# Kernel optimization log

Measured on AMD Instinct MI355X. Metric: run time of the kernel, lower is better.

The kernel has to match this reference:

```python
import jax, jax.numpy as jnp
import numpy as np

B, N, C, H, NC, P = 16, 577, 768, 12, 8, 576  # batch, seq(=patches+cls), dim, heads, curves, patches
D = C // H


def setup_inputs() -> dict:
    key = jax.random.key(0)
    ks = jax.random.split(key, 8)
    x = jax.random.normal(ks[0], (B, N, C), jnp.float32)
    qkv_w = jax.random.normal(ks[1], (C, 3 * C), jnp.float32) * 0.02
    proj_w = jax.random.normal(ks[2], (C, C), jnp.float32) * 0.02
    proj_b = jnp.zeros((C,), jnp.float32)
    # learned per-head decay logits; +3 so sigmoid ~0.95 (slow decay, realistic)
    ai_list = jax.random.normal(ks[3], (NC, H), jnp.float32) + 3.0
    mask_weights = jax.random.normal(ks[4], (NC,), jnp.float32) * 0.1 + 1.0 / NC
    normalize = 1.0 + 0.1 * jax.random.normal(ks[5], (H,), jnp.float32)
    # space-filling-curve inverse index permutations (one per curve)
    curve_inds = jnp.stack([
        jax.random.permutation(jax.random.fold_in(ks[6], c), P) for c in range(NC)
    ]).astype(jnp.int32)
    return dict(x=x, qkv_w=qkv_w, proj_w=proj_w, proj_b=proj_b,
                ai_list=ai_list, mask_weights=mask_weights,
                normalize=normalize, curve_inds=curve_inds)


def _build_mask(ai_list, mask_weights, curve_inds):
    # sigmoid(a)^|i-j| gathered by the curve permutation == sigmoid(a)^|ind_i - ind_j|
    a = jax.nn.sigmoid(ai_list)                                  # [NC,H]
    ci = curve_inds.astype(jnp.float32)                          # [NC,P]
    diff = jnp.abs(ci[:, :, None] - ci[:, None, :])              # [NC,P,P]
    Mc = a[:, :, None, None] ** diff[:, None, :, :]              # [NC,H,P,P]
    Mp = jnp.einsum('c,chpq->hpq', mask_weights, Mc)             # weighted sum over curves
    # cls-token row/col: each curve contributes ones -> sum of weights
    sw = jnp.sum(mask_weights)
    M = jnp.pad(Mp, ((0, 0), (1, 0), (1, 0)))                    # [H,N,N]
    M = M.at[:, 0, :].set(sw)
    M = M.at[:, :, 0].set(sw)
    return M


def reference(x, qkv_w, proj_w, proj_b, ai_list, mask_weights, normalize, curve_inds):
    qkv = (x @ qkv_w).reshape(B, N, 3, H, D)
    q = jnp.transpose(qkv[:, :, 0], (0, 2, 1, 3))                # [B,H,N,D]
    k = jnp.transpose(qkv[:, :, 1], (0, 2, 1, 3))
    v = jnp.transpose(qkv[:, :, 2], (0, 2, 1, 3))
    # NOTE: original overwrites self.scale with the bool `scale`=True -> multiply by 1
    attn = jnp.einsum('bhnd,bhmd->bhnm', q, k)                   # [B,H,N,N]
    M = _build_mask(ai_list, mask_weights, curve_inds)           # [H,N,N]
    attn = attn * M[None] * normalize[None, :, None, None]       # method='mul_v1'
    attn = jax.nn.softmax(attn, axis=-1)
    out = jnp.einsum('bhnm,bhmd->bhnd', attn, v)
    out = jnp.transpose(out, (0, 2, 1, 3)).reshape(B, N, C)
    return out @ proj_w + proj_b
```

## Files before the change

### kernel.cpp

```cpp
#include <hip/hip_runtime.h>


typedef _Float16 f16;
typedef _Float16 half8 __attribute__((ext_vector_type(8)));
typedef _Float16 half4 __attribute__((ext_vector_type(4)));
typedef float floatx4 __attribute__((ext_vector_type(4)));

#define DEVINL __device__ __forceinline__

#define Bb 16
#define NN 577
#define CC 768
#define HH 12
#define DD 64
#define MM (Bb * NN)
#define VTLD 584
#define MLD 580
#define CLD 136

DEVINL void async_copy16(void* lds, const void* g) {
  __builtin_amdgcn_global_load_lds(
      (const __attribute__((address_space(1))) void*)g,
      (__attribute__((address_space(3))) void*)lds, 16, 0, 0);
}

DEVINL half8 ld_swz(const f16* lds, int row, int chunk) {
  return *(const half8*)(lds + row * 64 + ((chunk ^ (row & 7)) << 3));
}

DEVINL int xcd_swizzle(int orig, int nwg) {
  int q = nwg >> 3, r = nwg & 7;
  int xcd = orig & 7, loc = orig >> 3;
  return (xcd < r ? xcd * (q + 1) : r * (q + 1) + (xcd - r) * q) + loc;
}

__global__ void cvt_kernel(const float* __restrict__ in, f16* __restrict__ out, int n) {
  int i = (blockIdx.x * blockDim.x + threadIdx.x) * 4;
  if (i >= n) return;
  float4 v = *(const float4*)(in + i);
  half4 o = {(f16)v.x, (f16)v.y, (f16)v.z, (f16)v.w};
  *(half4*)(out + i) = o;
}

__global__ void transpose_cvt(const float* __restrict__ in, f16* __restrict__ out,
                              int N3, int K) {
  __shared__ float t[32][33];
  const int k0 = blockIdx.x * 32, n0 = blockIdx.y * 32;
  const int tx = threadIdx.x & 31, ty = threadIdx.x >> 5;
#pragma unroll
  for (int p = 0; p < 4; ++p)
    t[ty + p * 8][tx] = in[(size_t)(k0 + ty + p * 8) * N3 + n0 + tx];
  __syncthreads();
#pragma unroll
  for (int p = 0; p < 4; ++p)
    out[(size_t)(n0 + ty + p * 8) * K + k0 + tx] = (f16)t[tx][ty + p * 8];
}

__global__ void mask_kernel(const float* __restrict__ ai, const float* __restrict__ mw,
                            const float* __restrict__ nrm, const int* __restrict__ ci,
                            float* __restrict__ Mb) {
  const int i = blockIdx.x;
  const int h = blockIdx.y;
  __shared__ float la_s[8], wv_s[8], cif[8], swn_s;
  int tid = threadIdx.x;
  if (tid < 8) {
    float av = ai[tid * 12 + h];
    float a = 1.f / (1.f + __expf(-av));
    la_s[tid] = __logf(a);
    wv_s[tid] = mw[tid];
    cif[tid] = (i > 0) ? (float)ci[tid * 576 + (i - 1)] : 0.f;
  }
  if (tid == 0) {
    float s = 0.f;
    for (int c = 0; c < 8; ++c) s += mw[c];
    swn_s = s * nrm[h] * 1.44269504088896f;
  }
  __syncthreads();
  const float nr = nrm[h] * 1.44269504088896f;
  float* row = Mb + ((size_t)h * NN + i) * MLD;
  for (int j = tid; j < NN; j += blockDim.x) {
    float val;
    if (i == 0 || j == 0) {
      val = swn_s;
    } else {
      float acc = 0.f;
#pragma unroll
      for (int c = 0; c < 8; ++c) {
        float d = fabsf(cif[c] - (float)ci[c * 576 + (j - 1)]);
        acc += wv_s[c] * __expf(la_s[c] * d);
      }
      val = acc * nr;
    }
    row[j] = val;
  }
}

DEVINL void gemm_mainloop(const f16* __restrict__ A, const f16* __restrict__ Bt,
                          int arow0, int brow0, int maxar,
                          f16* SMEM, floatx4 acc[4][4], int tid) {
  const int lane = tid & 63;
  const int wid = tid >> 6;
  const int wr = wid >> 1, wc = wid & 1;
  const int l15 = lane & 15, g = lane >> 4;
  const int r_ = tid >> 3, cp_ = tid & 7;
  const int lc_ = (cp_ ^ (r_ & 7)) << 3;

  auto stage = [&](f16* As, f16* Bs, int k0) {
#pragma unroll
    for (int q = 0; q < 4; ++q) {
      int idx = q * 256 + tid;
      int r = q * 32 + r_;
      int ar = arow0 + r; if (ar > maxar) ar = maxar;
      async_copy16(As + idx * 8, A + (size_t)ar * CC + k0 + lc_);
      async_copy16(Bs + idx * 8, Bt + (size_t)(brow0 + r) * CC + k0 + lc_);
    }
  };
  auto compute = [&](const f16* As, const f16* Bs) {
#pragma unroll
    for (int kk = 0; kk < 2; ++kk) {
      half8 af[4], bf[4];
#pragma unroll
      for (int mi = 0; mi < 4; ++mi) af[mi] = ld_swz(As, wr * 64 + mi * 16 + l15, kk * 4 + g);
#pragma unroll
      for (int ni = 0; ni < 4; ++ni) bf[ni] = ld_swz(Bs, wc * 64 + ni * 16 + l15, kk * 4 + g);
#pragma unroll
      for (int mi = 0; mi < 4; ++mi)
#pragma unroll
        for (int ni = 0; ni < 4; ++ni)
          acc[mi][ni] = __builtin_amdgcn_mfma_f32_16x16x32_f16(af[mi], bf[ni], acc[mi][ni], 0, 0, 0);
    }
  };

  const int nt = CC / 64;
  stage(SMEM, SMEM + 8192, 0);
#pragma unroll 1
  for (int t = 0; t < nt; ++t) {
    f16* cAs = (t & 1) ? SMEM + 16384 : SMEM;
    f16* cBs = (t & 1) ? SMEM + 24576 : SMEM + 8192;
    f16* nAs = (t & 1) ? SMEM : SMEM + 16384;
    f16* nBs = (t & 1) ? SMEM + 8192 : SMEM + 24576;
    if (t + 1 < nt) {
      stage(nAs, nBs, (t + 1) * 64);
      asm volatile("s_waitcnt vmcnt(8)" ::: "memory");
    } else {
      asm volatile("s_waitcnt vmcnt(0)" ::: "memory");
    }
    __builtin_amdgcn_s_barrier();
    __builtin_amdgcn_sched_barrier(0);
    compute(cAs, cBs);
    __builtin_amdgcn_s_barrier();
  }
}

__global__ __launch_bounds__(256, 2)
void gemm_qkv(const f16* __restrict__ A, const f16* __restrict__ Bt,
              f16* __restrict__ qb, f16* __restrict__ kb, f16* __restrict__ vt) {
  __shared__ __align__(16) f16 SMEM[32768];
  floatx4 acc[4][4] = {};
  const int nwg = 18 * 73;
  const int wgid = xcd_swizzle(blockIdx.y * gridDim.x + blockIdx.x, nwg);
  const int m0 = (wgid / 18) * 128, n0 = (wgid % 18) * 128;
  gemm_mainloop(A, Bt, m0, n0, MM - 1, SMEM, acc, threadIdx.x);
  const int tid = threadIdx.x, lane = tid & 63, wid = tid >> 6;
  const int wr = wid >> 1, wc = wid & 1, l15 = lane & 15, g = lane >> 4;
  const int t = n0 / CC;
  const int h0 = (n0 - t * CC) >> 6;
  if (t < 2) {
#pragma unroll
    for (int mi = 0; mi < 4; ++mi)
#pragma unroll
      for (int ni = 0; ni < 4; ++ni)
#pragma unroll
        for (int r = 0; r < 4; ++r)
          SMEM[(wr * 64 + mi * 16 + 4 * g + r) * CLD + wc * 64 + ni * 16 + l15] =
              (f16)acc[mi][ni][r];
    __syncthreads();
    f16* dst = (t == 0) ? qb : kb;
#pragma unroll
    for (int p = 0; p < 8; ++p) {
      int c = p * 256 + tid;
      int ml = c >> 4, n3c = (c & 15) << 3;
      int mg = m0 + ml;
      if (mg < MM) {
        int b = mg / NN, n = mg - b * NN;
        int h = h0 + (n3c >> 6), d0 = n3c & 63;
        half8 v = *(const half8*)(SMEM + ml * CLD + n3c);
        *(half8*)(dst + ((size_t)(b * HH + h) * NN + n) * DD + d0) = v;
      }
    }
  } else {
#pragma unroll
    for (int mi = 0; mi < 4; ++mi)
#pragma unroll
      for (int ni = 0; ni < 4; ++ni)
#pragma unroll
        for (int r = 0; r < 4; ++r)
          SMEM[(wc * 64 + ni * 16 + l15) * CLD + wr * 64 + mi * 16 + 4 * g + r] =
              (f16)acc[mi][ni][r];
    __syncthreads();
#pragma unroll
    for (int p = 0; p < 8; ++p) {
      int c = p * 256 + tid;
      int n3 = c >> 4, mc = (c & 15) << 3;
      int mg = m0 + mc;
      int h = h0 + (n3 >> 6), d = n3 & 63;
      half8 v = *(const half8*)(SMEM + n3 * CLD + mc);
      int b0 = mg / NN, b7 = (mg + 7) / NN;
      if (mg + 7 < MM && b0 == b7) {
        *(half8*)(vt + ((size_t)(b0 * HH + h) * DD + d) * VTLD + (mg - b0 * NN)) = v;
      } else {
#pragma unroll
        for (int e = 0; e < 8; ++e) {
          int m2 = mg + e;
          if (m2 < MM) {
            int b = m2 / NN;
            vt[((size_t)(b * HH + h) * DD + d) * VTLD + (m2 - b * NN)] = v[e];
          }
        }
      }
    }
  }
}

__global__ __launch_bounds__(256, 2)
void gemm_proj(const f16* __restrict__ A, const f16* __restrict__ Bt,
               const float* __restrict__ bias, float* __restrict__ out) {
  __shared__ __align__(16) f16 SMEM[32768];
  floatx4 acc[4][4] = {};
  const int nwg = 6 * 73;
  const int wgid = xcd_swizzle(blockIdx.y * gridDim.x + blockIdx.x, nwg);
  const int m0 = (wgid / 6) * 128, n0 = (wgid % 6) * 128;
  gemm_mainloop(A, Bt, m0, n0, MM - 1, SMEM, acc, threadIdx.x);
  const int lane = threadIdx.x & 63, wid = threadIdx.x >> 6;
  const int wr = wid >> 1, wc = wid & 1, l15 = lane & 15, g = lane >> 4;
#pragma unroll
  for (int mi = 0; mi < 4; ++mi)
#pragma unroll
    for (int ni = 0; ni < 4; ++ni)
#pragma unroll
      for (int r = 0; r < 4; ++r) {
        int m = m0 + wr * 64 + mi * 16 + 4 * g + r;
        if (m >= MM) continue;
        int n = n0 + wc * 64 + ni * 16 + l15;
        out[(size_t)m * CC + n] = acc[mi][ni][r] + bias[n];
      }
}

__global__ __launch_bounds__(256, 2)
void attn_kernel(const f16* __restrict__ qb, const f16* __restrict__ kb,
                 const f16* __restrict__ vt, const float* __restrict__ Mb,
                 f16* __restrict__ aout) {
  __shared__ f16 Ks[2][64 * 64];
  __shared__ f16 Vs[2][64 * 64];
  const int D0 = (blockIdx.z * gridDim.y + blockIdx.y) * gridDim.x + blockIdx.x;
  const int wgid = xcd_swizzle(D0, 5 * HH * Bb);
  const int it = wgid % 5;
  const int rem = wgid / 5;
  const int b = rem % Bb, h = rem / Bb;
  const int tid = threadIdx.x, lane = tid & 63, wid = tid >> 6;
  const int l15 = lane & 15, g = lane >> 4;
  const size_t bh = (size_t)b * HH + h;
  const f16* qbh = qb + bh * NN * DD;
  const f16* kbh = kb + bh * NN * DD;
  const f16* vbh = vt + bh * DD * VTLD;
  const float* Mh = Mb + (size_t)h * NN * MLD;
  const int row0w = it * 128 + wid * 32;

  half8 qB[2][2];
#pragma unroll
  for (int qt = 0; qt < 2; ++qt) {
    int qr = row0w + qt * 16 + l15; if (qr > NN - 1) qr = NN - 1;
    const f16* qp = qbh + (size_t)qr * DD + g * 8;
    qB[qt][0] = *(const half8*)qp;
    qB[qt][1] = *(const half8*)(qp + 32);
  }
  const float* Mrow0;
  const float* Mrow1;
  {
    int r0 = row0w + l15;      if (r0 > NN - 1) r0 = NN - 1;
    int r1 = row0w + 16 + l15; if (r1 > NN - 1) r1 = NN - 1;
    Mrow0 = Mh + (size_t)r0 * MLD + 4 * g;
    Mrow1 = Mh + (size_t)r1 * MLD + 4 * g;
  }

  floatx4 acc[2][4] = {};
  float lsum[2] = {0.f, 0.f};
  float mrun[2] = {-3e38f, -3e38f};

  auto stage = [&](f16* Kd, f16* Vd, int j0) {
#pragma unroll
    for (int qi = 0; qi < 2; ++qi) {
      int idx = qi * 256 + tid;
      int r = idx >> 3, cp = idx & 7;
      int lc = (cp ^ (r & 7)) << 3;
      int j = j0 + r; if (j > NN - 1) j = NN - 1;
      async_copy16(Kd + idx * 8, kbh + (size_t)j * DD + lc);
      async_copy16(Vd + idx * 8, vbh + (size_t)r * VTLD + j0 + lc);
    }
  };
  auto ldmask = [&](floatx4 m4[2][4], int j0) {
#pragma unroll
    for (int jt = 0; jt < 4; ++jt) {
      m4[0][jt] = *(const floatx4*)(Mrow0 + j0 + jt * 16);
      m4[1][jt] = *(const floatx4*)(Mrow1 + j0 + jt * 16);
    }
  };
  auto compute = [&](const f16* Kc, const f16* Vc, floatx4 m4[2][4], int j0) {
    floatx4 sf[2][4];
#pragma unroll
    for (int jt = 0; jt < 4; ++jt) {
      half8 ka0 = ld_swz(Kc, jt * 16 + l15, g);
      half8 ka1 = ld_swz(Kc, jt * 16 + l15, 4 + g);
#pragma unroll
      for (int qt = 0; qt < 2; ++qt) {
        floatx4 z = {0.f, 0.f, 0.f, 0.f};
        z = __builtin_amdgcn_mfma_f32_16x16x32_f16(ka0, qB[qt][0], z, 0, 0, 0);
        z = __builtin_amdgcn_mfma_f32_16x16x32_f16(ka1, qB[qt][1], z, 0, 0, 0);
        sf[qt][jt] = z;
      }
    }
#pragma unroll
    for (int qt = 0; qt < 2; ++qt)
#pragma unroll
      for (int jt = 0; jt < 4; ++jt)
#pragma unroll
        for (int r = 0; r < 4; ++r) sf[qt][jt][r] *= m4[qt][jt][r];
    if (j0 + 64 > NN) {
#pragma unroll
      for (int qt = 0; qt < 2; ++qt)
#pragma unroll
        for (int jt = 0; jt < 4; ++jt)
#pragma unroll
          for (int r = 0; r < 4; ++r)
            if (j0 + jt * 16 + 4 * g + r >= NN) sf[qt][jt][r] = -3e38f;
    }
    half4 pB[2][4];
#pragma unroll
    for (int qt = 0; qt < 2; ++qt) {
      float pj[4];
#pragma unroll
      for (int jt = 0; jt < 4; ++jt)
        pj[jt] = fmaxf(fmaxf(sf[qt][jt][0], sf[qt][jt][1]),
                       fmaxf(sf[qt][jt][2], sf[qt][jt][3]));
      float pmax = fmaxf(fmaxf(pj[0], pj[1]), fmaxf(pj[2], pj[3]));
      pmax = fmaxf(pmax, __shfl_xor(pmax, 16));
      pmax = fmaxf(pmax, __shfl_xor(pmax, 32));
      if (!__all(pmax - mrun[qt] <= 8.f)) {
        float mnew = fmaxf(mrun[qt], pmax);
        float fac = __builtin_amdgcn_exp2f(mrun[qt] - mnew);
        mrun[qt] = mnew;
        lsum[qt] *= fac;
#pragma unroll
        for (int dt = 0; dt < 4; ++dt)
#pragma unroll
          for (int r = 0; r < 4; ++r) acc[qt][dt][r] *= fac;
      }
      float lsj[4];
#pragma unroll
      for (int jt = 0; jt < 4; ++jt) {
        half4 pb;
        float p0 = __builtin_amdgcn_exp2f(sf[qt][jt][0] - mrun[qt]);
        float p1 = __builtin_amdgcn_exp2f(sf[qt][jt][1] - mrun[qt]);
        float p2 = __builtin_amdgcn_exp2f(sf[qt][jt][2] - mrun[qt]);
        float p3 = __builtin_amdgcn_exp2f(sf[qt][jt][3] - mrun[qt]);
        pb[0] = (f16)p0; pb[1] = (f16)p1; pb[2] = (f16)p2; pb[3] = (f16)p3;
        lsj[jt] = (p0 + p1) + (p2 + p3);
        pB[qt][jt] = pb;
      }
      lsum[qt] += (lsj[0] + lsj[1]) + (lsj[2] + lsj[3]);
    }
#pragma unroll
    for (int dt = 0; dt < 4; ++dt)
#pragma unroll
      for (int jt = 0; jt < 4; ++jt) {
        int c16 = (jt * 2 + (g >> 1)) ^ (l15 & 7);
        half4 va = *(const half4*)(Vc + (dt * 16 + l15) * 64 + (c16 << 3) + (g & 1) * 4);
#pragma unroll
        for (int qt = 0; qt < 2; ++qt)
          acc[qt][dt] = __builtin_amdgcn_mfma_f32_16x16x16f16(va, pB[qt][jt], acc[qt][dt], 0, 0, 0);
      }
  };

  floatx4 m4A[2][4], m4B[2][4];
  stage(Ks[0], Vs[0], 0);
  ldmask(m4A, 0);

#pragma unroll 1
  for (int t = 0; t < 10; t += 2) {
    ldmask(m4B, (t + 1) * 64);
    asm volatile("s_waitcnt vmcnt(8)" ::: "memory");
    __builtin_amdgcn_s_barrier();
    __builtin_amdgcn_sched_barrier(0);
    stage(Ks[1], Vs[1], (t + 1) * 64);
    compute(Ks[0], Vs[0], m4A, t * 64);
    const int j2 = (t + 2 < 10) ? (t + 2) * 64 : 0;
    ldmask(m4A, j2);
    asm volatile("s_waitcnt vmcnt(8)" ::: "memory");
    __builtin_amdgcn_s_barrier();
    __builtin_amdgcn_sched_barrier(0);
    stage(Ks[0], Vs[0], j2);
    compute(Ks[1], Vs[1], m4B, (t + 1) * 64);
  }

#pragma unroll
  for (int qt = 0; qt < 2; ++qt) {
    float v = lsum[qt];
    v += __shfl_xor(v, 16);
    v += __shfl_xor(v, 32);
    float linv = 1.f / v;
    int n = row0w + qt * 16 + l15;
    if (n < NN) {
#pragma unroll
      for (int dt = 0; dt < 4; ++dt) {
        half4 o;
#pragma unroll
        for (int r = 0; r < 4; ++r) o[r] = (f16)(acc[qt][dt][r] * linv);
        *(half4*)(aout + ((size_t)(b * NN + n)) * CC + h * DD + dt * 16 + 4 * g) = o;
      }
    }
  }
}

extern "C" void kernel_launch(void* const* d_in, const int* in_sizes, int n_in,
                              void* d_out, int out_size, void* d_ws, size_t ws_size,
                              hipStream_t stream) {
  const float* x    = (const float*)d_in[0];
  const float* qkvw = (const float*)d_in[1];
  const float* pw   = (const float*)d_in[2];
  const float* pb   = (const float*)d_in[3];
  const float* ai   = (const float*)d_in[4];
  const float* mw   = (const float*)d_in[5];
  const float* nrm  = (const float*)d_in[6];
  const int*   ci   = (const int*)d_in[7];
  float* out = (float*)d_out;

  char* wsb = (char*)d_ws;
  size_t off = 0;
  auto alloc = [&](size_t bytes) {
    char* p = wsb + off;
    off += (bytes + 255) & ~(size_t)255;
    return p;
  };
  f16*   x_h  = (f16*)alloc((size_t)MM * CC * 2);
  f16*   w_t  = (f16*)alloc((size_t)3 * CC * CC * 2);
  f16*   pw_t = (f16*)alloc((size_t)CC * CC * 2);
  float* Mb   = (float*)alloc((size_t)HH * NN * MLD * 4 + 1024);
  f16*   qb   = (f16*)alloc((size_t)Bb * HH * NN * DD * 2);
  f16*   kb   = (f16*)alloc((size_t)Bb * HH * NN * DD * 2);
  f16*   vt   = (f16*)alloc((size_t)Bb * HH * DD * VTLD * 2);
  (void)alloc(4096);
  f16* aout = x_h;

  cvt_kernel<<<(MM * CC / 4 + 255) / 256, 256, 0, stream>>>(x, x_h, MM * CC);
  transpose_cvt<<<dim3(CC / 32, 3 * CC / 32), 256, 0, stream>>>(qkvw, w_t, 3 * CC, CC);
  transpose_cvt<<<dim3(CC / 32, CC / 32), 256, 0, stream>>>(pw, pw_t, CC, CC);
  mask_kernel<<<dim3(NN, HH), 256, 0, stream>>>(ai, mw, nrm, ci, Mb);
  gemm_qkv<<<dim3(18, 73), 256, 0, stream>>>(x_h, w_t, qb, kb, vt);
  attn_kernel<<<dim3(5, HH, Bb), 256, 0, stream>>>(qb, kb, vt, Mb, aout);
  gemm_proj<<<dim3(6, 73), 256, 0, stream>>>(aout, pw_t, pb, out);
}
```

Baseline: 163.1 us.

## Use 8 waves of 16 query rows per attention block instead of 4 waves of 32

The attention kernel now launches 512 threads per block, and each wave handles a single 16-row query tile instead of two. This cuts per-wave register use (accumulators, score tiles, mask values) so more waves can be resident, and staging drops to one async copy per thread per matrix. In exchange each K/V tile read from LDS is reused by only one query tile per wave, raising LDS traffic per MFMA, and barrier cost grows with the larger block.

Result: faster. 159.4 us (-2.3%).

```diff
diff --git a/kernel.cpp b/kernel.cpp
--- a/kernel.cpp
+++ b/kernel.cpp
@@ -246,7 +246,7 @@
       }
 }
 
-__global__ __launch_bounds__(256, 2)
+__global__ __launch_bounds__(512, 4)
 void attn_kernel(const f16* __restrict__ qb, const f16* __restrict__ kb,
                  const f16* __restrict__ vt, const float* __restrict__ Mb,
                  f16* __restrict__ aout) {
@@ -264,157 +264,133 @@
   const f16* kbh = kb + bh * NN * DD;
   const f16* vbh = vt + bh * DD * VTLD;
   const float* Mh = Mb + (size_t)h * NN * MLD;
-  const int row0w = it * 128 + wid * 32;
-
-  half8 qB[2][2];
-#pragma unroll
-  for (int qt = 0; qt < 2; ++qt) {
-    int qr = row0w + qt * 16 + l15; if (qr > NN - 1) qr = NN - 1;
+  const int row0w = it * 128 + wid * 16;
+
+  half8 qB0, qB1;
+  {
+    int qr = row0w + l15; if (qr > NN - 1) qr = NN - 1;
     const f16* qp = qbh + (size_t)qr * DD + g * 8;
-    qB[qt][0] = *(const half8*)qp;
-    qB[qt][1] = *(const half8*)(qp + 32);
-  }
-  const float* Mrow0;
-  const float* Mrow1;
+    qB0 = *(const half8*)qp;
+    qB1 = *(const half8*)(qp + 32);
+  }
+  const float* Mrow;
   {
-    int r0 = row0w + l15;      if (r0 > NN - 1) r0 = NN - 1;
-    int r1 = row0w + 16 + l15; if (r1 > NN - 1) r1 = NN - 1;
-    Mrow0 = Mh + (size_t)r0 * MLD + 4 * g;
-    Mrow1 = Mh + (size_t)r1 * MLD + 4 * g;
-  }
-
-  floatx4 acc[2][4] = {};
-  float lsum[2] = {0.f, 0.f};
-  float mrun[2] = {-3e38f, -3e38f};
-
+    int r0 = row0w + l15; if (r0 > NN - 1) r0 = NN - 1;
+    Mrow = Mh + (size_t)r0 * MLD + 4 * g;
+  }
+
+  floatx4 acc[4] = {};
+  float lsum = 0.f;
+  float mrun = -3e38f;
+
+  const int sr_ = tid >> 3, scp_ = tid & 7;
+  const int slc_ = (scp_ ^ (sr_ & 7)) << 3;
   auto stage = [&](f16* Kd, f16* Vd, int j0) {
-#pragma unroll
-    for (int qi = 0; qi < 2; ++qi) {
-      int idx = qi * 256 + tid;
-      int r = idx >> 3, cp = idx & 7;
-      int lc = (cp ^ (r & 7)) << 3;
-      int j = j0 + r; if (j > NN - 1) j = NN - 1;
-      async_copy16(Kd + idx * 8, kbh + (size_t)j * DD + lc);
-      async_copy16(Vd + idx * 8, vbh + (size_t)r * VTLD + j0 + lc);
-    }
-  };
-  auto ldmask = [&](floatx4 m4[2][4], int j0) {
-#pragma unroll
-    for (int jt = 0; jt < 4; ++jt) {
-      m4[0][jt] = *(const floatx4*)(Mrow0 + j0 + jt * 16);
-      m4[1][jt] = *(const floatx4*)(Mrow1 + j0 + jt * 16);
-    }
-  };
-  auto compute = [&](const f16* Kc, const f16* Vc, floatx4 m4[2][4], int j0) {
-    floatx4 sf[2][4];
+    int j = j0 + sr_; if (j > NN - 1) j = NN - 1;
+    async_copy16(Kd + tid * 8, kbh + (size_t)j * DD + slc_);
+    async_copy16(Vd + tid * 8, vbh + (size_t)sr_ * VTLD + j0 + slc_);
+  };
+  auto ldmask = [&](floatx4 m4[4], int j0) {
+#pragma unroll
+    for (int jt = 0; jt < 4; ++jt)
+      m4[jt] = *(const floatx4*)(Mrow + j0 + jt * 16);
+  };
+  auto compute = [&](const f16* Kc, const f16* Vc, floatx4 m4[4], int j0) {
+    floatx4 sf[4];
 #pragma unroll
     for (int jt = 0; jt < 4; ++jt) {
       half8 ka0 = ld_swz(Kc, jt * 16 + l15, g);
       half8 ka1 = ld_swz(Kc, jt * 16 + l15, 4 + g);
-#pragma unroll
-      for (int qt = 0; qt < 2; ++qt) {
-        floatx4 z = {0.f, 0.f, 0.f, 0.f};
-        z = __builtin_amdgcn_mfma_f32_16x16x32_f16(ka0, qB[qt][0], z, 0, 0, 0);
-        z = __builtin_amdgcn_mfma_f32_16x16x32_f16(ka1, qB[qt][1], z, 0, 0, 0);
-        sf[qt][jt] = z;
-      }
-    }
-#pragma unroll
-    for (int qt = 0; qt < 2; ++qt)
+      floatx4 z = {0.f, 0.f, 0.f, 0.f};
+      z = __builtin_amdgcn_mfma_f32_16x16x32_f16(ka0, qB0, z, 0, 0, 0);
+      z = __builtin_amdgcn_mfma_f32_16x16x32_f16(ka1, qB1, z, 0, 0, 0);
+      sf[jt] = z;
+    }
+#pragma unroll
+    for (int jt = 0; jt < 4; ++jt)
+#pragma unroll
+      for (int r = 0; r < 4; ++r) sf[jt][r] *= m4[jt][r];
+    if (j0 + 64 > NN) {
 #pragma unroll
       for (int jt = 0; jt < 4; ++jt)
 #pragma unroll
-        for (int r = 0; r < 4; ++r) sf[qt][jt][r] *= m4[qt][jt][r];
-    if (j0 + 64 > NN) {
-#pragma unroll
-      for (int qt = 0; qt < 2; ++qt)
-#pragma unroll
-        for (int jt = 0; jt < 4; ++jt)
-#pragma unroll
-          for (int r = 0; r < 4; ++r)
-            if (j0 + jt * 16 + 4 * g + r >= NN) sf[qt][jt][r] = -3e38f;
-    }
-    half4 pB[2][4];
-#pragma unroll
-    for (int qt = 0; qt < 2; ++qt) {
-      float pj[4];
-#pragma unroll
-      for (int jt = 0; jt < 4; ++jt)
-        pj[jt] = fmaxf(fmaxf(sf[qt][jt][0], sf[qt][jt][1]),
-                       fmaxf(sf[qt][jt][2], sf[qt][jt][3]));
-      float pmax = fmaxf(fmaxf(pj[0], pj[1]), fmaxf(pj[2], pj[3]));
-      pmax = fmaxf(pmax, __shfl_xor(pmax, 16));
-      pmax = fmaxf(pmax, __shfl_xor(pmax, 32));
-      if (!__all(pmax - mrun[qt] <= 8.f)) {
-        float mnew = fmaxf(mrun[qt], pmax);
-        float fac = __builtin_amdgcn_exp2f(mrun[qt] - mnew);
-        mrun[qt] = mnew;
-        lsum[qt] *= fac;
-#pragma unroll
-        for (int dt = 0; dt < 4; ++dt)
-#pragma unroll
-          for (int r = 0; r < 4; ++r) acc[qt][dt][r] *= fac;
-      }
-      float lsj[4];
-#pragma unroll
-      for (int jt = 0; jt < 4; ++jt) {
-        half4 pb;
-        float p0 = __builtin_amdgcn_exp2f(sf[qt][jt][0] - mrun[qt]);
-        float p1 = __builtin_amdgcn_exp2f(sf[qt][jt][1] - mrun[qt]);
-        float p2 = __builtin_amdgcn_exp2f(sf[qt][jt][2] - mrun[qt]);
-        float p3 = __builtin_amdgcn_exp2f(sf[qt][jt][3] - mrun[qt]);
-        pb[0] = (f16)p0; pb[1] = (f16)p1; pb[2] = (f16)p2; pb[3] = (f16)p3;
-        lsj[jt] = (p0 + p1) + (p2 + p3);
-        pB[qt][jt] = pb;
-      }
-      lsum[qt] += (lsj[0] + lsj[1]) + (lsj[2] + lsj[3]);
-    }
+        for (int r = 0; r < 4; ++r)
+          if (j0 + jt * 16 + 4 * g + r >= NN) sf[jt][r] = -3e38f;
+    }
+    float pj[4];
+#pragma unroll
+    for (int jt = 0; jt < 4; ++jt)
+      pj[jt] = fmaxf(fmaxf(sf[jt][0], sf[jt][1]), fmaxf(sf[jt][2], sf[jt][3]));
+    float pmax = fmaxf(fmaxf(pj[0], pj[1]), fmaxf(pj[2], pj[3]));
+    pmax = fmaxf(pmax, __shfl_xor(pmax, 16));
+    pmax = fmaxf(pmax, __shfl_xor(pmax, 32));
+    if (!__all(pmax - mrun <= 8.f)) {
+      float mnew = fmaxf(mrun, pmax);
+      float fac = __builtin_amdgcn_exp2f(mrun - mnew);
+      mrun = mnew;
+      lsum *= fac;
+#pragma unroll
+      for (int dt = 0; dt < 4; ++dt)
+#pragma unroll
+        for (int r = 0; r < 4; ++r) acc[dt][r] *= fac;
+    }
+    half4 pB[4];
+    float lsj[4];
+#pragma unroll
+    for (int jt = 0; jt < 4; ++jt) {
+      half4 pb;
+      float p0 = __builtin_amdgcn_exp2f(sf[jt][0] - mrun);
+      float p1 = __builtin_amdgcn_exp2f(sf[jt][1] - mrun);
+      float p2 = __builtin_amdgcn_exp2f(sf[jt][2] - mrun);
+      float p3 = __builtin_amdgcn_exp2f(sf[jt][3] - mrun);
+      pb[0] = (f16)p0; pb[1] = (f16)p1; pb[2] = (f16)p2; pb[3] = (f16)p3;
+      lsj[jt] = (p0 + p1) + (p2 + p3);
+      pB[jt] = pb;
+    }
+    lsum += (lsj[0] + lsj[1]) + (lsj[2] + lsj[3]);
 #pragma unroll
     for (int dt = 0; dt < 4; ++dt)
 #pragma unroll
       for (int jt = 0; jt < 4; ++jt) {
         int c16 = (jt * 2 + (g >> 1)) ^ (l15 & 7);
         half4 va = *(const half4*)(Vc + (dt * 16 + l15) * 64 + (c16 << 3) + (g & 1) * 4);
-#pragma unroll
-        for (int qt = 0; qt < 2; ++qt)
-          acc[qt][dt] = __builtin_amdgcn_mfma_f32_16x16x16f16(va, pB[qt][jt], acc[qt][dt], 0, 0, 0);
-      }
-  };
-
-  floatx4 m4A[2][4], m4B[2][4];
+        acc[dt] = __builtin_amdgcn_mfma_f32_16x16x16f16(va, pB[jt], acc[dt], 0, 0, 0);
+      }
+  };
+
+  floatx4 m4A[4], m4B[4];
   stage(Ks[0], Vs[0], 0);
   ldmask(m4A, 0);
 
 #pragma unroll 1
   for (int t = 0; t < 10; t += 2) {
     ldmask(m4B, (t + 1) * 64);
-    asm volatile("s_waitcnt vmcnt(8)" ::: "memory");
+    asm volatile("s_waitcnt vmcnt(4)" ::: "memory");
     __builtin_amdgcn_s_barrier();
     __builtin_amdgcn_sched_barrier(0);
     stage(Ks[1], Vs[1], (t + 1) * 64);
     compute(Ks[0], Vs[0], m4A, t * 64);
     const int j2 = (t + 2 < 10) ? (t + 2) * 64 : 0;
     ldmask(m4A, j2);
-    asm volatile("s_waitcnt vmcnt(8)" ::: "memory");
+    asm volatile("s_waitcnt vmcnt(4)" ::: "memory");
     __builtin_amdgcn_s_barrier();
     __builtin_amdgcn_sched_barrier(0);
     stage(Ks[0], Vs[0], j2);
     compute(Ks[1], Vs[1], m4B, (t + 1) * 64);
   }
 
-#pragma unroll
-  for (int qt = 0; qt < 2; ++qt) {
-    float v = lsum[qt];
+  {
+    float v = lsum;
     v += __shfl_xor(v, 16);
     v += __shfl_xor(v, 32);
     float linv = 1.f / v;
-    int n = row0w + qt * 16 + l15;
+    int n = row0w + l15;
     if (n < NN) {
 #pragma unroll
       for (int dt = 0; dt < 4; ++dt) {
         half4 o;
 #pragma unroll
-        for (int r = 0; r < 4; ++r) o[r] = (f16)(acc[qt][dt][r] * linv);
+        for (int r = 0; r < 4; ++r) o[r] = (f16)(acc[dt][r] * linv);
         *(half4*)(aout + ((size_t)(b * NN + n)) * CC + h * DD + dt * 16 + 4 * g) = o;
       }
     }
@@ -456,6 +432,6 @@
   transpose_cvt<<<dim3(CC / 32, CC / 32), 256, 0, stream>>>(pw, pw_t, CC, CC);
   mask_kernel<<<dim3(NN, HH), 256, 0, stream>>>(ai, mw, nrm, ci, Mb);
   gemm_qkv<<<dim3(18, 73), 256, 0, stream>>>(x_h, w_t, qb, kb, vt);
-  attn_kernel<<<dim3(5, HH, Bb), 256, 0, stream>>>(qb, kb, vt, Mb, aout);
+  attn_kernel<<<dim3(5, HH, Bb), 512, 0, stream>>>(qb, kb, vt, Mb, aout);
   gemm_proj<<<dim3(6, 73), 256, 0, stream>>>(aout, pw_t, pb, out);
 }
```
